# Optimization experiments

Measured on AMD Instinct MI355X. Metric: run time of the kernel, lower is better.

The kernel has to match this reference:

```python
import jax, jax.numpy as jnp
import numpy as np

N = 100000
E = 600000
IN_DIM = 128
HID = 128


def setup_inputs() -> dict:
    key = jax.random.key(0)
    ks = jax.random.split(key, 12)
    def lin(kw, fan_in, fan_out):
        # torch nn.Linear default init: U(-1/sqrt(fan_in), 1/sqrt(fan_in))
        bound = 1.0 / np.sqrt(fan_in)
        kw1, kw2 = jax.random.split(kw)
        w = jax.random.uniform(kw1, (fan_in, fan_out), jnp.float32, -bound, bound)
        b = jax.random.uniform(kw2, (fan_out,), jnp.float32, -bound, bound)
        return w, b
    x = jax.random.normal(ks[0], (N, IN_DIM), jnp.float32)
    edge_index = jax.random.randint(ks[1], (2, E), 0, N, jnp.int64)
    w1a, b1a = lin(ks[2], IN_DIM, HID)
    w1b, b1b = lin(ks[3], HID, HID)
    w2a, b2a = lin(ks[4], HID, HID)
    w2b, b2b = lin(ks[5], HID, HID)
    wo, bo = lin(ks[6], HID, 1)
    return {"x": x, "edge_index": edge_index,
            "w1a": w1a, "b1a": b1a, "w1b": w1b, "b1b": b1b,
            "w2a": w2a, "b2a": b2a, "w2b": w2b, "b2b": b2b,
            "wo": wo, "bo": bo}


def _gin_conv(x, src, dst, wa, ba, wb, bb):
    # sum-aggregate neighbor features: agg[dst] += x[src]; eps = 0 (GIN default)
    agg = jax.ops.segment_sum(x[src], dst, num_segments=N)
    h = x + agg
    h = jax.nn.relu(h @ wa + ba)
    return h @ wb + bb


def reference(x, edge_index, w1a, b1a, w1b, b1b, w2a, b2a, w2b, b2b, wo, bo):
    src, dst = edge_index[0], edge_index[1]
    h = _gin_conv(x, src, dst, w1a, b1a, w1b, b1b)
    h = _gin_conv(h, src, dst, w2a, b2a, w2b, b2b)
    return (h @ wo + bo).squeeze(-1)  # [N]
```

## Files before the change

### kernel.cpp

```cpp
#include <hip/hip_runtime.h>

typedef unsigned short u16;
typedef unsigned int u32;
typedef __bf16 bf16x8 __attribute__((ext_vector_type(8)));
typedef float f32x4 __attribute__((ext_vector_type(4)));

#define CAP 32

__device__ __forceinline__ u16 f2bf(float f) {
  union { float f; u32 u; } c; c.f = f;
  return (u16)((c.u + 0x7fffu + ((c.u >> 16) & 1u)) >> 16);
}
__device__ __forceinline__ float2 upk2(u32 v) {
  union { u32 u; float f; } a, b; a.u = v << 16; b.u = v & 0xffff0000u;
  return make_float2(a.f, b.f);
}
__device__ __forceinline__ u32 pk2(float x, float y) {
  return (u32)f2bf(x) | ((u32)f2bf(y) << 16);
}
__device__ __forceinline__ void fma8u(float* acc, uint4 v, float w) {
  float2 p;
  p = upk2(v.x); acc[0] = fmaf(w, p.x, acc[0]); acc[1] = fmaf(w, p.y, acc[1]);
  p = upk2(v.y); acc[2] = fmaf(w, p.x, acc[2]); acc[3] = fmaf(w, p.y, acc[3]);
  p = upk2(v.z); acc[4] = fmaf(w, p.x, acc[4]); acc[5] = fmaf(w, p.y, acc[5]);
  p = upk2(v.w); acc[6] = fmaf(w, p.x, acc[6]); acc[7] = fmaf(w, p.y, acc[7]);
}

__global__ __launch_bounds__(256) void k_prep2(const float4* __restrict__ x4,
                                               uint2* __restrict__ xb,
                                               int n4, int castBlocks, int trBlocks,
                                               const float* __restrict__ w0,
                                               const float* __restrict__ w1,
                                               const float* __restrict__ w2,
                                               const float* __restrict__ w3,
                                               u16* __restrict__ wT,
                                               int* __restrict__ cursor, int N) {
  int b = blockIdx.x, t = threadIdx.x;
  if (b < castBlocks) {
    int i = b * 256 + t;
    if (i < n4) {
      float4 v = x4[i];
      xb[i] = make_uint2(pk2(v.x, v.y), pk2(v.z, v.w));
    }
  } else if (b < castBlocks + trBlocks) {
    int id = (b - castBlocks) * 256 + t;
    int w = id >> 14, rem = id & 16383;
    int nn = rem >> 7, kk = rem & 127;
    const float* s = (w == 0) ? w0 : (w == 1) ? w1 : (w == 2) ? w2 : w3;
    wT[id] = f2bf(s[kk * 128 + nn]);
  } else {
    int i = (b - castBlocks - trBlocks) * 256 + t;
    if (i < N) cursor[i] = 0;
  }
}

__global__ __launch_bounds__(256) void k_fillp(const int* __restrict__ src,
                                               const int* __restrict__ dst,
                                               int* __restrict__ cursor,
                                               int* __restrict__ edge_src, int E) {
  int e = blockIdx.x * 256 + threadIdx.x;
  if (e < E) {
    int d = dst[e];
    int pos = atomicAdd(&cursor[d], 1);
    if (pos < CAP) edge_src[d * CAP + pos] = src[e];
  }
}

template <bool HEAD>
__global__ __launch_bounds__(256) void k_mlp(const u16* __restrict__ in,
                                             const int* __restrict__ cursor,
                                             const int* __restrict__ edge_src,
                                             const u16* __restrict__ wAT,
                                             const float* __restrict__ bA,
                                             const u16* __restrict__ wBT,
                                             const float* __restrict__ bB,
                                             const float* __restrict__ wo,
                                             const float* __restrict__ bo,
                                             void* __restrict__ outp,
                                             int N, int ntiles) {
  __shared__ u16 lA[64 * 128];
  __shared__ u16 lW[2 * 128 * 128];
  const int tid = threadIdx.x;
  const int wave = tid >> 6, lane = tid & 63;
  const int m16 = lane & 15, quad = lane >> 4;
  const uint4* in4 = (const uint4*)in;

#pragma unroll
  for (int it = 0; it < 16; ++it) {
    int id = it * 256 + tid;
    int m = id >> 11, rem = id & 2047;
    int row = rem >> 4, c = rem & 15;
    const u16* s = m ? wBT : wAT;
    uint4 v = *(const uint4*)&s[row * 128 + c * 8];
    *(uint4*)&lW[m * 16384 + row * 128 + ((c ^ (row & 15)) << 3)] = v;
  }

  float bAr[8], bBr[8], woR[8], bBh[8];
#pragma unroll
  for (int t = 0; t < 8; ++t) {
    bAr[t] = bA[t * 16 + m16];
    bBr[t] = HEAD ? 0.f : bB[t * 16 + m16];
    woR[t] = HEAD ? wo[t * 16 + m16] : 0.f;
    bBh[t] = HEAD ? bB[t * 16 + m16] : 0.f;
  }
  float boV = HEAD ? bo[0] : 0.f;

  __syncthreads();

  const int mrow = wave * 16 + m16;

  uint4 pf[4];
  int2 eL[4]; int cntL[4]; uint4 svL[4];

  auto aissue = [&](int tl) {
#pragma unroll
    for (int it = 0; it < 4; ++it) {
      int node = tl * 64 + wave * 16 + it * 4 + quad;
      int nc = node < N ? node : N - 1;
      eL[it] = *(const int2*)&edge_src[nc * CAP + 2 * m16];
      cntL[it] = cursor[nc];
      svL[it] = in4[(size_t)nc * 16 + m16];
    }
  };

  auto gi = [&](int it, int cnt, uint4* v) {
#pragma unroll
    for (int k = 0; k < 8; ++k) {
      int idx = __shfl((k & 1) ? eL[it].y : eL[it].x, (quad << 4) + (k >> 1), 64);
      uint4 vv = make_uint4(0u, 0u, 0u, 0u);
      if (k < cnt) vv = in4[(size_t)idx * 16 + m16];
      v[k] = vv;
    }
  };
  auto gc = [&](int it, int cnt, uint4* v, bool valid) {
    float a8[8];
#pragma unroll
    for (int i = 0; i < 8; ++i) a8[i] = 0.f;
    fma8u(a8, svL[it], valid ? 1.f : 0.f);
#pragma unroll
    for (int k = 0; k < 8; ++k) fma8u(a8, v[k], 1.f);
    for (int b = 8; b < cnt; b += 8) {
      uint4 w[8];
#pragma unroll
      for (int k = 0; k < 8; ++k) {
        int idx = __shfl((k & 1) ? eL[it].y : eL[it].x, (quad << 4) + (b >> 1) + (k >> 1), 64);
        uint4 vv = make_uint4(0u, 0u, 0u, 0u);
        if (b + k < cnt) vv = in4[(size_t)idx * 16 + m16];
        w[k] = vv;
      }
#pragma unroll
      for (int k = 0; k < 8; ++k) fma8u(a8, w[k], 1.f);
    }
    pf[it] = make_uint4(pk2(a8[0], a8[1]), pk2(a8[2], a8[3]),
                        pk2(a8[4], a8[5]), pk2(a8[6], a8[7]));
  };

  auto aconsume = [&](int tl) {
    int base = tl * 64 + wave * 16 + quad;
    bool v0 = base + 0 < N, v1 = base + 4 < N, v2 = base + 8 < N, v3 = base + 12 < N;
    int c0 = v0 ? (cntL[0] < CAP ? cntL[0] : CAP) : 0;
    int c1 = v1 ? (cntL[1] < CAP ? cntL[1] : CAP) : 0;
    int c2 = v2 ? (cntL[2] < CAP ? cntL[2] : CAP) : 0;
    int c3 = v3 ? (cntL[3] < CAP ? cntL[3] : CAP) : 0;
    uint4 vA[8], vB[8];
    gi(0, c0, vA);
    gi(1, c1, vB);
    gc(0, c0, vA, v0);
    gi(2, c2, vA);
    gc(1, c1, vB, v1);
    gi(3, c3, vB);
    gc(2, c2, vA, v2);
    gc(3, c3, vB, v3);
  };

  int tile = blockIdx.x;
  if (tile < ntiles) { aissue(tile); aconsume(tile); }
  for (; tile < ntiles; tile += gridDim.x) {
#pragma unroll
    for (int it = 0; it < 4; ++it) {
      int row = wave * 16 + it * 4 + quad;
      *(uint4*)&lA[row * 128 + ((m16 ^ (row & 15)) << 3)] = pf[it];
    }
    bf16x8 aF[4];
#pragma unroll
    for (int ks = 0; ks < 4; ++ks)
      aF[ks] = *(const bf16x8*)&lA[mrow * 128 + (((ks * 4 + quad) ^ m16) << 3)];
    int nxt = tile + gridDim.x;
    if (nxt < ntiles) aissue(nxt);

    f32x4 acc[8];
#pragma unroll
    for (int t = 0; t < 8; ++t) acc[t] = (f32x4){0.f, 0.f, 0.f, 0.f};
#pragma unroll
    for (int t = 0; t < 8; ++t) {
      int nrow = t * 16 + m16;
#pragma unroll
      for (int ks = 0; ks < 4; ++ks) {
        bf16x8 bF = *(const bf16x8*)&lW[nrow * 128 + (((ks * 4 + quad) ^ m16) << 3)];
        acc[t] = __builtin_amdgcn_mfma_f32_16x16x32_bf16(aF[ks], bF, acc[t], 0, 0, 0);
      }
    }
#pragma unroll
    for (int t = 0; t < 8; ++t) {
      int n = t * 16 + m16;
#pragma unroll
      for (int r = 0; r < 4; ++r) {
        int rloc = quad * 4 + r;
        int absrow = wave * 16 + rloc;
        float v = acc[t][r] + bAr[t];
        v = v > 0.f ? v : 0.f;
        lA[absrow * 128 + ((((n >> 3) ^ rloc) << 3) | (n & 7))] = f2bf(v);
      }
    }
#pragma unroll
    for (int ks = 0; ks < 4; ++ks)
      aF[ks] = *(const bf16x8*)&lA[mrow * 128 + (((ks * 4 + quad) ^ m16) << 3)];
#pragma unroll
    for (int t = 0; t < 8; ++t) acc[t] = (f32x4){0.f, 0.f, 0.f, 0.f};
#pragma unroll
    for (int t = 0; t < 8; ++t) {
      int nrow = t * 16 + m16;
#pragma unroll
      for (int ks = 0; ks < 4; ++ks) {
        bf16x8 bF = *(const bf16x8*)&lW[16384 + nrow * 128 + (((ks * 4 + quad) ^ m16) << 3)];
        acc[t] = __builtin_amdgcn_mfma_f32_16x16x32_bf16(aF[ks], bF, acc[t], 0, 0, 0);
      }
    }
    if (!HEAD) {
#pragma unroll
      for (int t = 0; t < 8; ++t) {
        int n = t * 16 + m16;
#pragma unroll
        for (int r = 0; r < 4; ++r) {
          int rloc = quad * 4 + r;
          int absrow = wave * 16 + rloc;
          float v = acc[t][r] + bBr[t];
          lA[absrow * 128 + ((((n >> 3) ^ rloc) << 3) | (n & 7))] = f2bf(v);
        }
      }
      u16* out = (u16*)outp;
#pragma unroll
      for (int it = 0; it < 4; ++it) {
        int row = wave * 16 + it * 4 + quad;
        int gr = tile * 64 + row;
        if (gr < N) {
          uint4 v = *(const uint4*)&lA[row * 128 + ((m16 ^ (row & 15)) << 3)];
          *(uint4*)&out[(size_t)gr * 128 + m16 * 8] = v;
        }
      }
    } else {
      float* out = (float*)outp;
      float s[4];
#pragma unroll
      for (int r = 0; r < 4; ++r) {
        float v = 0.f;
#pragma unroll
        for (int t = 0; t < 8; ++t) v += (acc[t][r] + bBh[t]) * woR[t];
        s[r] = v;
      }
#pragma unroll
      for (int r = 0; r < 4; ++r) {
        s[r] += __shfl_xor(s[r], 1, 64);
        s[r] += __shfl_xor(s[r], 2, 64);
        s[r] += __shfl_xor(s[r], 4, 64);
        s[r] += __shfl_xor(s[r], 8, 64);
      }
      if (m16 == 0) {
#pragma unroll
        for (int r = 0; r < 4; ++r) {
          int gr = tile * 64 + wave * 16 + quad * 4 + r;
          if (gr < N) out[gr] = s[r] + boV;
        }
      }
    }
    if (nxt < ntiles) aconsume(nxt);
  }
}

extern "C" void kernel_launch(void* const* d_in, const int* in_sizes, int n_in,
                              void* d_out, int out_size, void* d_ws, size_t ws_size,
                              hipStream_t stream) {
  const float* x = (const float*)d_in[0];
  const int* ei = (const int*)d_in[1];
  const int E = in_sizes[1] / 2;
  const int N = in_sizes[0] / 128;
  const int* srcI = ei;
  const int* dstI = ei + E;
  const float* w1a = (const float*)d_in[2];
  const float* b1a = (const float*)d_in[3];
  const float* w1b = (const float*)d_in[4];
  const float* b1b = (const float*)d_in[5];
  const float* w2a = (const float*)d_in[6];
  const float* b2a = (const float*)d_in[7];
  const float* w2b = (const float*)d_in[8];
  const float* b2b = (const float*)d_in[9];
  const float* wo = (const float*)d_in[10];
  const float* bo = (const float*)d_in[11];

  char* ws = (char*)d_ws;
  size_t off = 0;
  auto nx = [&](size_t bytes) {
    size_t o = off;
    off += (bytes + 511) & ~(size_t)511;
    return o;
  };
  int* cursor   = (int*)(ws + nx((size_t)N * 4));
  int* edge_src = (int*)(ws + nx((size_t)N * CAP * 4));
  u16* wT       = (u16*)(ws + nx((size_t)4 * 16384 * 2));
  u16* xb       = (u16*)(ws + nx((size_t)N * 128 * 2));
  u16* bufB     = (u16*)(ws + nx((size_t)N * 128 * 2));

  const int n4 = N * 32;
  const int castBlocks = (n4 + 255) / 256;
  const int trBlocks = 256;
  const int zeroBlocks = (N + 255) / 256;

  k_prep2<<<castBlocks + trBlocks + zeroBlocks, 256, 0, stream>>>(
      (const float4*)x, (uint2*)xb, n4, castBlocks, trBlocks,
      w1a, w1b, w2a, w2b, wT, cursor, N);
  k_fillp<<<(E + 255) / 256, 256, 0, stream>>>(srcI, dstI, cursor, edge_src, E);

  const int ntiles = (N + 63) / 64;
  const int mlpGrid = 512;

  k_mlp<false><<<mlpGrid, 256, 0, stream>>>(xb, cursor, edge_src,
                                            wT, b1a, wT + 16384, b1b,
                                            nullptr, nullptr, bufB, N, ntiles);
  k_mlp<true><<<mlpGrid, 256, 0, stream>>>(bufB, cursor, edge_src,
                                           wT + 32768, b2a, wT + 49152, b2b,
                                           wo, bo, d_out, N, ntiles);
}
```

Before: 231.7 us.

## Schedule 16-node chunks per wave via atomic work queue and interleave gathers with MFMA

Replaces the static grid-stride 64-row tile loop with per-wave dynamic scheduling: each wave grabs 16-node chunks from a global atomic counter (one per layer, zeroed in the prep kernel). The next chunk's neighbor gathers and accumulations are split and interleaved between the two MFMA GEMM phases and the epilogue, so gather latency overlaps tensor-core work. The aim is to balance the irregular degree distribution across waves and hide memory latency. It adds an atomic per chunk and more register pressure from keeping the vA/vB gather buffers live across the GEMMs.

```diff
diff --git a/kernel.cpp b/kernel.cpp
--- a/kernel.cpp
+++ b/kernel.cpp
@@ -34,7 +34,8 @@
                                                const float* __restrict__ w2,
                                                const float* __restrict__ w3,
                                                u16* __restrict__ wT,
-                                               int* __restrict__ cursor, int N) {
+                                               int* __restrict__ cursor,
+                                               int* __restrict__ ctr, int N) {
   int b = blockIdx.x, t = threadIdx.x;
   if (b < castBlocks) {
     int i = b * 256 + t;
@@ -51,6 +52,7 @@
   } else {
     int i = (b - castBlocks - trBlocks) * 256 + t;
     if (i < N) cursor[i] = 0;
+    if (b == castBlocks + trBlocks && t < 2) ctr[t] = 0;
   }
 }
 
@@ -77,7 +79,7 @@
                                              const float* __restrict__ wo,
                                              const float* __restrict__ bo,
                                              void* __restrict__ outp,
-                                             int N, int ntiles) {
+                                             int N, int nch, int* __restrict__ ctr) {
   __shared__ u16 lA[64 * 128];
   __shared__ u16 lW[2 * 128 * 128];
   const int tid = threadIdx.x;
@@ -111,11 +113,12 @@
 
   uint4 pf[4];
   int2 eL[4]; int cntL[4]; uint4 svL[4];
-
-  auto aissue = [&](int tl) {
+  uint4 vA[8], vB[8];
+
+  auto aissue = [&](int c) {
 #pragma unroll
     for (int it = 0; it < 4; ++it) {
-      int node = tl * 64 + wave * 16 + it * 4 + quad;
+      int node = c * 16 + it * 4 + quad;
       int nc = node < N ? node : N - 1;
       eL[it] = *(const int2*)&edge_src[nc * CAP + 2 * m16];
       cntL[it] = cursor[nc];
@@ -155,27 +158,31 @@
                         pk2(a8[4], a8[5]), pk2(a8[6], a8[7]));
   };
 
-  auto aconsume = [&](int tl) {
-    int base = tl * 64 + wave * 16 + quad;
-    bool v0 = base + 0 < N, v1 = base + 4 < N, v2 = base + 8 < N, v3 = base + 12 < N;
-    int c0 = v0 ? (cntL[0] < CAP ? cntL[0] : CAP) : 0;
-    int c1 = v1 ? (cntL[1] < CAP ? cntL[1] : CAP) : 0;
-    int c2 = v2 ? (cntL[2] < CAP ? cntL[2] : CAP) : 0;
-    int c3 = v3 ? (cntL[3] < CAP ? cntL[3] : CAP) : 0;
-    uint4 vA[8], vB[8];
-    gi(0, c0, vA);
-    gi(1, c1, vB);
-    gc(0, c0, vA, v0);
-    gi(2, c2, vA);
-    gc(1, c1, vB, v1);
-    gi(3, c3, vB);
-    gc(2, c2, vA, v2);
-    gc(3, c3, vB, v3);
-  };
-
-  int tile = blockIdx.x;
-  if (tile < ntiles) { aissue(tile); aconsume(tile); }
-  for (; tile < ntiles; tile += gridDim.x) {
+  int cur;
+  if (lane == 0) cur = atomicAdd(ctr, 1);
+  cur = __shfl(cur, 0);
+  if (cur < nch) {
+    aissue(cur);
+    int base = cur * 16 + quad;
+    bool y0 = base < N, y1 = base + 4 < N, y2 = base + 8 < N, y3 = base + 12 < N;
+    int d0 = y0 ? (cntL[0] < CAP ? cntL[0] : CAP) : 0;
+    int d1 = y1 ? (cntL[1] < CAP ? cntL[1] : CAP) : 0;
+    int d2 = y2 ? (cntL[2] < CAP ? cntL[2] : CAP) : 0;
+    int d3 = y3 ? (cntL[3] < CAP ? cntL[3] : CAP) : 0;
+    gi(0, d0, vA); gi(1, d1, vB);
+    gc(0, d0, vA, y0); gi(2, d2, vA);
+    gc(1, d1, vB, y1); gi(3, d3, vB);
+    gc(2, d2, vA, y2); gc(3, d3, vB, y3);
+  }
+  int nxt;
+  if (lane == 0) nxt = atomicAdd(ctr, 1);
+  nxt = __shfl(nxt, 0);
+  if (nxt < nch) aissue(nxt);
+
+  while (cur < nch) {
+    int fut = 0;
+    if (lane == 0) fut = atomicAdd(ctr, 1);
+
 #pragma unroll
     for (int it = 0; it < 4; ++it) {
       int row = wave * 16 + it * 4 + quad;
@@ -185,8 +192,6 @@
 #pragma unroll
     for (int ks = 0; ks < 4; ++ks)
       aF[ks] = *(const bf16x8*)&lA[mrow * 128 + (((ks * 4 + quad) ^ m16) << 3)];
-    int nxt = tile + gridDim.x;
-    if (nxt < ntiles) aissue(nxt);
 
     f32x4 acc[8];
 #pragma unroll
@@ -200,6 +205,21 @@
         acc[t] = __builtin_amdgcn_mfma_f32_16x16x32_bf16(aF[ks], bF, acc[t], 0, 0, 0);
       }
     }
+
+    bool hn = nxt < nch;
+    int nb = nxt * 16 + quad;
+    bool w0 = false, w1 = false, w2 = false, w3 = false;
+    int c0 = 0, c1 = 0, c2 = 0, c3 = 0;
+    if (hn) {
+      w0 = nb < N; w1 = nb + 4 < N; w2 = nb + 8 < N; w3 = nb + 12 < N;
+      c0 = w0 ? (cntL[0] < CAP ? cntL[0] : CAP) : 0;
+      c1 = w1 ? (cntL[1] < CAP ? cntL[1] : CAP) : 0;
+      c2 = w2 ? (cntL[2] < CAP ? cntL[2] : CAP) : 0;
+      c3 = w3 ? (cntL[3] < CAP ? cntL[3] : CAP) : 0;
+      gi(0, c0, vA);
+      gi(1, c1, vB);
+    }
+
 #pragma unroll
     for (int t = 0; t < 8; ++t) {
       int n = t * 16 + m16;
@@ -226,6 +246,12 @@
         acc[t] = __builtin_amdgcn_mfma_f32_16x16x32_bf16(aF[ks], bF, acc[t], 0, 0, 0);
       }
     }
+
+    if (hn) {
+      gc(0, c0, vA, w0); gi(2, c2, vA);
+      gc(1, c1, vB, w1); gi(3, c3, vB);
+    }
+
     if (!HEAD) {
 #pragma unroll
       for (int t = 0; t < 8; ++t) {
@@ -242,7 +268,7 @@
 #pragma unroll
       for (int it = 0; it < 4; ++it) {
         int row = wave * 16 + it * 4 + quad;
-        int gr = tile * 64 + row;
+        int gr = cur * 16 + it * 4 + quad;
         if (gr < N) {
           uint4 v = *(const uint4*)&lA[row * 128 + ((m16 ^ (row & 15)) << 3)];
           *(uint4*)&out[(size_t)gr * 128 + m16 * 8] = v;
@@ -268,12 +294,20 @@
       if (m16 == 0) {
 #pragma unroll
         for (int r = 0; r < 4; ++r) {
-          int gr = tile * 64 + wave * 16 + quad * 4 + r;
+          int gr = cur * 16 + quad * 4 + r;
           if (gr < N) out[gr] = s[r] + boV;
         }
       }
     }
-    if (nxt < ntiles) aconsume(nxt);
+
+    if (hn) {
+      gc(2, c2, vA, w2);
+      gc(3, c3, vB, w3);
+    }
+
+    cur = nxt;
+    nxt = __shfl(fut, 0);
+    if (nxt < nch) aissue(nxt);
   }
 }
 
@@ -304,6 +338,7 @@
     off += (bytes + 511) & ~(size_t)511;
     return o;
   };
+  int* ctr      = (int*)(ws + nx(8));
   int* cursor   = (int*)(ws + nx((size_t)N * 4));
   int* edge_src = (int*)(ws + nx((size_t)N * CAP * 4));
   u16* wT       = (u16*)(ws + nx((size_t)4 * 16384 * 2));
@@ -317,16 +352,16 @@
 
   k_prep2<<<castBlocks + trBlocks + zeroBlocks, 256, 0, stream>>>(
       (const float4*)x, (uint2*)xb, n4, castBlocks, trBlocks,
-      w1a, w1b, w2a, w2b, wT, cursor, N);
+      w1a, w1b, w2a, w2b, wT, cursor, ctr, N);
   k_fillp<<<(E + 255) / 256, 256, 0, stream>>>(srcI, dstI, cursor, edge_src, E);
 
-  const int ntiles = (N + 63) / 64;
+  const int nch = (N + 15) / 16;
   const int mlpGrid = 512;
 
   k_mlp<false><<<mlpGrid, 256, 0, stream>>>(xb, cursor, edge_src,
                                             wT, b1a, wT + 16384, b1b,
-                                            nullptr, nullptr, bufB, N, ntiles);
+                                            nullptr, nullptr, bufB, N, nch, ctr);
   k_mlp<true><<<mlpGrid, 256, 0, stream>>>(bufB, cursor, edge_src,
                                            wT + 32768, b2a, wT + 49152, b2b,
-                                           wo, bo, d_out, N, ntiles);
-}
+                                           wo, bo, d_out, N, nch, ctr + 1);
+}
```

Measured after the change: 387.4 us. 67.2% more time.

## Split MLP kernel into producer gather waves and consumer MFMA waves

Applied to the files above, without the earlier changes.

The kernel is restructured into warp specialization. Waves 0-1 gather and aggregate neighbor rows for the next tile (8 nodes per lane group). Waves 2-3 run the two-layer MFMA MLP on the current tile from a shared buffer, with block barriers handing tiles off between the two groups. The aim is to overlap the latency-bound gather with tensor-core compute. In exchange, only half the waves gather and half compute, register pressure per producer goes up, and there are two __syncthreads per tile.

```diff
diff --git a/kernel.cpp b/kernel.cpp
--- a/kernel.cpp
+++ b/kernel.cpp
@@ -78,8 +78,8 @@
                                              const float* __restrict__ bo,
                                              void* __restrict__ outp,
                                              int N, int ntiles) {
-  __shared__ u16 lA[64 * 128];
   __shared__ u16 lW[2 * 128 * 128];
+  __shared__ u16 hbuf[64 * 128];
   const int tid = threadIdx.x;
   const int wave = tid >> 6, lane = tid & 63;
   const int m16 = lane & 15, quad = lane >> 4;
@@ -105,45 +105,44 @@
   }
   float boV = HEAD ? bo[0] : 0.f;
 
-  __syncthreads();
-
-  const int mrow = wave * 16 + m16;
-
-  uint4 pf[4];
-  int2 eL[4]; int cntL[4]; uint4 svL[4];
+  const bool isProd = wave < 2;
+  const int pw = wave;
+  const int cw = wave - 2;
+
+  int2 eL[8]; int cntL[8]; uint4 svL[8]; uint4 pf[8];
+  uint4 vA[8], vB[8];
 
   auto aissue = [&](int tl) {
 #pragma unroll
-    for (int it = 0; it < 4; ++it) {
-      int node = tl * 64 + wave * 16 + it * 4 + quad;
+    for (int j = 0; j < 8; ++j) {
+      int node = tl * 64 + pw * 32 + quad * 8 + j;
       int nc = node < N ? node : N - 1;
-      eL[it] = *(const int2*)&edge_src[nc * CAP + 2 * m16];
-      cntL[it] = cursor[nc];
-      svL[it] = in4[(size_t)nc * 16 + m16];
-    }
-  };
-
-  auto gi = [&](int it, int cnt, uint4* v) {
+      eL[j] = *(const int2*)&edge_src[nc * CAP + 2 * m16];
+      cntL[j] = cursor[nc];
+      svL[j] = in4[(size_t)nc * 16 + m16];
+    }
+  };
+  auto gi = [&](int j, int cnt, uint4* v) {
 #pragma unroll
     for (int k = 0; k < 8; ++k) {
-      int idx = __shfl((k & 1) ? eL[it].y : eL[it].x, (quad << 4) + (k >> 1), 64);
+      int idx = __shfl((k & 1) ? eL[j].y : eL[j].x, (quad << 4) + (k >> 1), 64);
       uint4 vv = make_uint4(0u, 0u, 0u, 0u);
       if (k < cnt) vv = in4[(size_t)idx * 16 + m16];
       v[k] = vv;
     }
   };
-  auto gc = [&](int it, int cnt, uint4* v, bool valid) {
+  auto gc = [&](int j, int cnt, uint4* v, bool valid) {
     float a8[8];
 #pragma unroll
     for (int i = 0; i < 8; ++i) a8[i] = 0.f;
-    fma8u(a8, svL[it], valid ? 1.f : 0.f);
+    fma8u(a8, svL[j], valid ? 1.f : 0.f);
 #pragma unroll
     for (int k = 0; k < 8; ++k) fma8u(a8, v[k], 1.f);
     for (int b = 8; b < cnt; b += 8) {
       uint4 w[8];
 #pragma unroll
       for (int k = 0; k < 8; ++k) {
-        int idx = __shfl((k & 1) ? eL[it].y : eL[it].x, (quad << 4) + (b >> 1) + (k >> 1), 64);
+        int idx = __shfl((k & 1) ? eL[j].y : eL[j].x, (quad << 4) + (b >> 1) + (k >> 1), 64);
         uint4 vv = make_uint4(0u, 0u, 0u, 0u);
         if (b + k < cnt) vv = in4[(size_t)idx * 16 + m16];
         w[k] = vv;
@@ -151,129 +150,151 @@
 #pragma unroll
       for (int k = 0; k < 8; ++k) fma8u(a8, w[k], 1.f);
     }
-    pf[it] = make_uint4(pk2(a8[0], a8[1]), pk2(a8[2], a8[3]),
-                        pk2(a8[4], a8[5]), pk2(a8[6], a8[7]));
-  };
-
-  auto aconsume = [&](int tl) {
-    int base = tl * 64 + wave * 16 + quad;
-    bool v0 = base + 0 < N, v1 = base + 4 < N, v2 = base + 8 < N, v3 = base + 12 < N;
-    int c0 = v0 ? (cntL[0] < CAP ? cntL[0] : CAP) : 0;
-    int c1 = v1 ? (cntL[1] < CAP ? cntL[1] : CAP) : 0;
-    int c2 = v2 ? (cntL[2] < CAP ? cntL[2] : CAP) : 0;
-    int c3 = v3 ? (cntL[3] < CAP ? cntL[3] : CAP) : 0;
-    uint4 vA[8], vB[8];
-    gi(0, c0, vA);
-    gi(1, c1, vB);
-    gc(0, c0, vA, v0);
-    gi(2, c2, vA);
-    gc(1, c1, vB, v1);
-    gi(3, c3, vB);
-    gc(2, c2, vA, v2);
-    gc(3, c3, vB, v3);
-  };
-
-  int tile = blockIdx.x;
-  if (tile < ntiles) { aissue(tile); aconsume(tile); }
-  for (; tile < ntiles; tile += gridDim.x) {
-#pragma unroll
-    for (int it = 0; it < 4; ++it) {
-      int row = wave * 16 + it * 4 + quad;
-      *(uint4*)&lA[row * 128 + ((m16 ^ (row & 15)) << 3)] = pf[it];
-    }
-    bf16x8 aF[4];
-#pragma unroll
-    for (int ks = 0; ks < 4; ++ks)
-      aF[ks] = *(const bf16x8*)&lA[mrow * 128 + (((ks * 4 + quad) ^ m16) << 3)];
-    int nxt = tile + gridDim.x;
-    if (nxt < ntiles) aissue(nxt);
-
-    f32x4 acc[8];
-#pragma unroll
-    for (int t = 0; t < 8; ++t) acc[t] = (f32x4){0.f, 0.f, 0.f, 0.f};
-#pragma unroll
-    for (int t = 0; t < 8; ++t) {
-      int nrow = t * 16 + m16;
-#pragma unroll
-      for (int ks = 0; ks < 4; ++ks) {
-        bf16x8 bF = *(const bf16x8*)&lW[nrow * 128 + (((ks * 4 + quad) ^ m16) << 3)];
-        acc[t] = __builtin_amdgcn_mfma_f32_16x16x32_bf16(aF[ks], bF, acc[t], 0, 0, 0);
-      }
-    }
-#pragma unroll
-    for (int t = 0; t < 8; ++t) {
-      int n = t * 16 + m16;
-#pragma unroll
-      for (int r = 0; r < 4; ++r) {
-        int rloc = quad * 4 + r;
-        int absrow = wave * 16 + rloc;
-        float v = acc[t][r] + bAr[t];
-        v = v > 0.f ? v : 0.f;
-        lA[absrow * 128 + ((((n >> 3) ^ rloc) << 3) | (n & 7))] = f2bf(v);
-      }
-    }
-#pragma unroll
-    for (int ks = 0; ks < 4; ++ks)
-      aF[ks] = *(const bf16x8*)&lA[mrow * 128 + (((ks * 4 + quad) ^ m16) << 3)];
-#pragma unroll
-    for (int t = 0; t < 8; ++t) acc[t] = (f32x4){0.f, 0.f, 0.f, 0.f};
-#pragma unroll
-    for (int t = 0; t < 8; ++t) {
-      int nrow = t * 16 + m16;
-#pragma unroll
-      for (int ks = 0; ks < 4; ++ks) {
-        bf16x8 bF = *(const bf16x8*)&lW[16384 + nrow * 128 + (((ks * 4 + quad) ^ m16) << 3)];
-        acc[t] = __builtin_amdgcn_mfma_f32_16x16x32_bf16(aF[ks], bF, acc[t], 0, 0, 0);
-      }
-    }
-    if (!HEAD) {
+    pf[j] = make_uint4(pk2(a8[0], a8[1]), pk2(a8[2], a8[3]),
+                       pk2(a8[4], a8[5]), pk2(a8[6], a8[7]));
+  };
+  auto gatherTile = [&](int tl) {
+    int cc[8]; bool vr[8];
+#pragma unroll
+    for (int j = 0; j < 8; ++j) {
+      int node = tl * 64 + pw * 32 + quad * 8 + j;
+      vr[j] = node < N;
+      cc[j] = vr[j] ? (cntL[j] < CAP ? cntL[j] : CAP) : 0;
+    }
+    gi(0, cc[0], vA); gi(1, cc[1], vB);
+    gc(0, cc[0], vA, vr[0]); gi(2, cc[2], vA);
+    gc(1, cc[1], vB, vr[1]); gi(3, cc[3], vB);
+    gc(2, cc[2], vA, vr[2]); gi(4, cc[4], vA);
+    gc(3, cc[3], vB, vr[3]); gi(5, cc[5], vB);
+    gc(4, cc[4], vA, vr[4]); gi(6, cc[6], vA);
+    gc(5, cc[5], vB, vr[5]); gi(7, cc[7], vB);
+    gc(6, cc[6], vA, vr[6]);
+    gc(7, cc[7], vB, vr[7]);
+  };
+  auto writeTile = [&]() {
+#pragma unroll
+    for (int j = 0; j < 8; ++j) {
+      int row = pw * 32 + quad * 8 + j;
+      *(uint4*)&hbuf[row * 128 + ((m16 ^ (row & 15)) << 3)] = pf[j];
+    }
+  };
+
+  auto consume = [&](int tile) {
+#pragma unroll
+    for (int s = 0; s < 2; ++s) {
+      const int rbase = cw * 32 + s * 16;
+      const int mrow = rbase + m16;
+      bf16x8 aF[4];
+#pragma unroll
+      for (int ks = 0; ks < 4; ++ks)
+        aF[ks] = *(const bf16x8*)&hbuf[mrow * 128 + (((ks * 4 + quad) ^ m16) << 3)];
+      f32x4 acc[8];
+#pragma unroll
+      for (int t = 0; t < 8; ++t) acc[t] = (f32x4){0.f, 0.f, 0.f, 0.f};
+#pragma unroll
+      for (int t = 0; t < 8; ++t) {
+        int nrow = t * 16 + m16;
+#pragma unroll
+        for (int ks = 0; ks < 4; ++ks) {
+          bf16x8 bF = *(const bf16x8*)&lW[nrow * 128 + (((ks * 4 + quad) ^ m16) << 3)];
+          acc[t] = __builtin_amdgcn_mfma_f32_16x16x32_bf16(aF[ks], bF, acc[t], 0, 0, 0);
+        }
+      }
 #pragma unroll
       for (int t = 0; t < 8; ++t) {
         int n = t * 16 + m16;
 #pragma unroll
         for (int r = 0; r < 4; ++r) {
           int rloc = quad * 4 + r;
-          int absrow = wave * 16 + rloc;
-          float v = acc[t][r] + bBr[t];
-          lA[absrow * 128 + ((((n >> 3) ^ rloc) << 3) | (n & 7))] = f2bf(v);
-        }
-      }
+          int absrow = rbase + rloc;
+          float v = acc[t][r] + bAr[t];
+          v = v > 0.f ? v : 0.f;
+          hbuf[absrow * 128 + ((((n >> 3) ^ rloc) << 3) | (n & 7))] = f2bf(v);
+        }
+      }
+#pragma unroll
+      for (int ks = 0; ks < 4; ++ks)
+        aF[ks] = *(const bf16x8*)&hbuf[mrow * 128 + (((ks * 4 + quad) ^ m16) << 3)];
+#pragma unroll
+      for (int t = 0; t < 8; ++t) acc[t] = (f32x4){0.f, 0.f, 0.f, 0.f};
+#pragma unroll
+      for (int t = 0; t < 8; ++t) {
+        int nrow = t * 16 + m16;
+#pragma unroll
+        for (int ks = 0; ks < 4; ++ks) {
+          bf16x8 bF = *(const bf16x8*)&lW[16384 + nrow * 128 + (((ks * 4 + quad) ^ m16) << 3)];
+          acc[t] = __builtin_amdgcn_mfma_f32_16x16x32_bf16(aF[ks], bF, acc[t], 0, 0, 0);
+        }
+      }
+      if (!HEAD) {
+#pragma unroll
+        for (int t = 0; t < 8; ++t) {
+          int n = t * 16 + m16;
+#pragma unroll
+          for (int r = 0; r < 4; ++r) {
+            int rloc = quad * 4 + r;
+            int absrow = rbase + rloc;
+            float v = acc[t][r] + bBr[t];
+            hbuf[absrow * 128 + ((((n >> 3) ^ rloc) << 3) | (n & 7))] = f2bf(v);
+          }
+        }
+      } else {
+        float* out = (float*)outp;
+        float sv[4];
+#pragma unroll
+        for (int r = 0; r < 4; ++r) {
+          float v = 0.f;
+#pragma unroll
+          for (int t = 0; t < 8; ++t) v += (acc[t][r] + bBh[t]) * woR[t];
+          sv[r] = v;
+        }
+#pragma unroll
+        for (int r = 0; r < 4; ++r) {
+          sv[r] += __shfl_xor(sv[r], 1, 64);
+          sv[r] += __shfl_xor(sv[r], 2, 64);
+          sv[r] += __shfl_xor(sv[r], 4, 64);
+          sv[r] += __shfl_xor(sv[r], 8, 64);
+        }
+        if (m16 == 0) {
+#pragma unroll
+          for (int r = 0; r < 4; ++r) {
+            int gr = tile * 64 + rbase + quad * 4 + r;
+            if (gr < N) out[gr] = sv[r] + boV;
+          }
+        }
+      }
+    }
+    if (!HEAD) {
       u16* out = (u16*)outp;
 #pragma unroll
-      for (int it = 0; it < 4; ++it) {
-        int row = wave * 16 + it * 4 + quad;
+      for (int it = 0; it < 8; ++it) {
+        int row = cw * 32 + it * 4 + quad;
         int gr = tile * 64 + row;
         if (gr < N) {
-          uint4 v = *(const uint4*)&lA[row * 128 + ((m16 ^ (row & 15)) << 3)];
+          uint4 v = *(const uint4*)&hbuf[row * 128 + ((m16 ^ (row & 15)) << 3)];
           *(uint4*)&out[(size_t)gr * 128 + m16 * 8] = v;
         }
       }
+    }
+  };
+
+  int tile = blockIdx.x;
+  if (isProd && tile < ntiles) { aissue(tile); gatherTile(tile); }
+  __syncthreads();
+  if (isProd && tile < ntiles) writeTile();
+  __syncthreads();
+
+  for (; tile < ntiles;) {
+    int nxt = tile + gridDim.x;
+    if (isProd) {
+      if (nxt < ntiles) { aissue(nxt); gatherTile(nxt); }
     } else {
-      float* out = (float*)outp;
-      float s[4];
-#pragma unroll
-      for (int r = 0; r < 4; ++r) {
-        float v = 0.f;
-#pragma unroll
-        for (int t = 0; t < 8; ++t) v += (acc[t][r] + bBh[t]) * woR[t];
-        s[r] = v;
-      }
-#pragma unroll
-      for (int r = 0; r < 4; ++r) {
-        s[r] += __shfl_xor(s[r], 1, 64);
-        s[r] += __shfl_xor(s[r], 2, 64);
-        s[r] += __shfl_xor(s[r], 4, 64);
-        s[r] += __shfl_xor(s[r], 8, 64);
-      }
-      if (m16 == 0) {
-#pragma unroll
-        for (int r = 0; r < 4; ++r) {
-          int gr = tile * 64 + wave * 16 + quad * 4 + r;
-          if (gr < N) out[gr] = s[r] + boV;
-        }
-      }
-    }
-    if (nxt < ntiles) aconsume(nxt);
+      consume(tile);
+    }
+    __syncthreads();
+    if (isProd && nxt < ntiles) writeTile();
+    __syncthreads();
+    tile = nxt;
   }
 }
 
```

Result: slower. 304.9 us (+31.6%).
